# Performance work log

Measured on AMD Instinct MI355X. Metric: run time of the kernel, lower is better.

Reference implementation:

```python
import jax, jax.numpy as jnp
import numpy as np

D = 128
N = 20000
E = 640000
EPS = 1e-5


def setup_inputs() -> dict:
    key = jax.random.key(0)
    ks = jax.random.split(key, 12)
    x = jax.random.normal(ks[0], (N, D), dtype=jnp.float32)
    edge_index = jax.random.randint(ks[1], (2, E), 0, N, dtype=jnp.int64)
    edge_weight = jax.random.uniform(ks[2], (E,), dtype=jnp.float32)
    s = 1.0 / np.sqrt(D)
    # GraphConv params: lin_rel (bias=True) applied to aggregated messages,
    # lin_root (bias=False) applied to root features.
    W_rel = jax.random.uniform(ks[3], (D, D), minval=-s, maxval=s, dtype=jnp.float32)
    b_rel = jax.random.uniform(ks[4], (D,), minval=-s, maxval=s, dtype=jnp.float32)
    W_root = jax.random.uniform(ks[5], (D, D), minval=-s, maxval=s, dtype=jnp.float32)
    # add_linear Linear(out, out)
    lin_W = jax.random.uniform(ks[6], (D, D), minval=-s, maxval=s, dtype=jnp.float32)
    lin_b = jax.random.uniform(ks[7], (D,), minval=-s, maxval=s, dtype=jnp.float32)
    # LayerNorm affine params
    gamma = jnp.ones((D,), dtype=jnp.float32)
    beta = jnp.zeros((D,), dtype=jnp.float32)
    return {"x": x, "edge_index": edge_index, "edge_weight": edge_weight,
            "W_rel": W_rel, "b_rel": b_rel, "W_root": W_root,
            "lin_W": lin_W, "lin_b": lin_b, "gamma": gamma, "beta": beta}


def _layer_norm(h, gamma, beta):
    mu = jnp.mean(h, axis=-1, keepdims=True)
    var = jnp.mean(jnp.square(h - mu), axis=-1, keepdims=True)
    return (h - mu) * jax.lax.rsqrt(var + EPS) * gamma + beta


def reference(x, edge_index, edge_weight, W_rel, b_rel, W_root, lin_W, lin_b, gamma, beta):
    n = x.shape[0]
    src, dst = edge_index[0], edge_index[1]
    # message: edge_weight * x_j, gathered from source nodes
    msg = x[src] * edge_weight[:, None]                      # [E, D]
    # max aggregation to destination nodes; empty segments -> 0 (PyG fill)
    agg = jax.ops.segment_max(msg, dst, num_segments=n)      # [N, D]
    agg = jnp.where(jnp.isneginf(agg), 0.0, agg)
    # GraphConv: lin_rel(agg) + lin_root(x)
    h = agg @ W_rel.T + b_rel + x @ W_root.T                  # [N, D]
    # act + skip + norm
    h = jax.nn.gelu(h, approximate=False) + x
    h = _layer_norm(h, gamma, beta)
    # add_linear branch: act(lin(h)) + skip, then norm (module reuses self.norm)
    h2 = jax.nn.gelu(h @ lin_W.T + lin_b, approximate=False) + h
    h2 = _layer_norm(h2, gamma, beta)
    return h2, edge_weight
```

## Files before the change

### kernel.cpp

```cpp
#include <hip/hip_runtime.h>
#include <math.h>

#define N_NODES 20000
#define N_DIM   128
#define N_EDGES 640000
#define LN_EPS  1e-5f
#define CAP 64

#define TASK_E (N_EDGES / 4)
#define TASK_W 6144

typedef __attribute__((ext_vector_type(8))) short bf16x8;
typedef __attribute__((ext_vector_type(4))) float f32x4;

__device__ __forceinline__ float gelu_exact(float v) {
    return 0.5f * v * (1.0f + erff(v * 0.70710678118654752f));
}
__device__ __forceinline__ unsigned pack_bf16(float f) {
    unsigned b = __float_as_uint(f);
    return (b + 0x7FFFu + ((b >> 16) & 1u)) >> 16;
}
__device__ __forceinline__ bf16x8 pack8(const float* p) {
    union { bf16x8 v; unsigned short u[8]; } t;
    #pragma unroll
    for (int j = 0; j < 8; j++) t.u[j] = (unsigned short)pack_bf16(p[j]);
    return t.v;
}

__device__ __forceinline__ void pack_wfrag(int u, const float* __restrict__ Wr,
                                           const float* __restrict__ Wo,
                                           const float* __restrict__ Wl,
                                           unsigned short* __restrict__ Wb) {
    int m    = u >> 11;
    int rem  = u & 2047;
    int nt   = rem >> 8;
    int kt   = (rem >> 6) & 3;
    int lane = rem & 63;
    int n = nt * 16 + (lane & 15);
    int k = kt * 32 + ((lane >> 4) << 3);
    const float* W = (m == 0) ? Wr : ((m == 1) ? Wo : Wl);
    const float* p = W + n * N_DIM + k;
    union { uint4 q; unsigned short u16[8]; } t;
    #pragma unroll
    for (int j = 0; j < 8; j++) t.u16[j] = (unsigned short)pack_bf16(p[j]);
    ((uint4*)Wb)[u] = t.q;
}

__device__ __forceinline__ void gather_node(
    int node, int lane, const char* __restrict__ xb,
    int base, int dg, const int2* __restrict__ eb, unsigned* __restrict__ agg)
{
    const int lane8 = lane << 3;
    float m0 = -INFINITY, m1 = -INFINITY;
    const int hi = base + dg - 1;
    for (int j = 0; j < dg; j += 8) {
        int2 ev[8];
        #pragma unroll
        for (int k = 0; k < 8; k++)
            ev[k] = eb[min(base + j + k, hi)];
        float2 xv[8];
        #pragma unroll
        for (int k = 0; k < 8; k++)
            xv[k] = *(const float2*)(xb + (size_t)(unsigned)ev[k].x + lane8);
        #pragma unroll
        for (int k = 0; k < 8; k++) {
            float w = __int_as_float(ev[k].y);
            m0 = fmaxf(m0, xv[k].x * w);
            m1 = fmaxf(m1, xv[k].y * w);
        }
    }
    if (dg == 0) { m0 = 0.0f; m1 = 0.0f; }
    agg[node * 64 + lane] = pack_bf16(m0) | (pack_bf16(m1) << 16);
}

__global__ __launch_bounds__(256) void edge_pass_kernel(
    const int* __restrict__ ei, const float* __restrict__ ew,
    int* __restrict__ cnt, int2* __restrict__ buck, float* __restrict__ out_ew,
    const float* __restrict__ Wr, const float* __restrict__ Wo,
    const float* __restrict__ Wl, unsigned short* __restrict__ Wb)
{
    int t = blockIdx.x * blockDim.x + threadIdx.x;
    if (t < TASK_E) {
        int4 dst = ((const int4*)(ei + N_EDGES))[t];
        int4 src = ((const int4*)ei)[t];
        float4 w = ((const float4*)ew)[t];
        ((float4*)out_ew)[t] = w;
        int p0 = atomicAdd(&cnt[dst.x], 1);
        int p1 = atomicAdd(&cnt[dst.y], 1);
        int p2 = atomicAdd(&cnt[dst.z], 1);
        int p3 = atomicAdd(&cnt[dst.w], 1);
        buck[dst.x * CAP + min(p0, CAP - 1)] = make_int2(src.x << 9, __float_as_int(w.x));
        buck[dst.y * CAP + min(p1, CAP - 1)] = make_int2(src.y << 9, __float_as_int(w.y));
        buck[dst.z * CAP + min(p2, CAP - 1)] = make_int2(src.z << 9, __float_as_int(w.z));
        buck[dst.w * CAP + min(p3, CAP - 1)] = make_int2(src.w << 9, __float_as_int(w.w));
    } else if (t < TASK_E + TASK_W) {
        pack_wfrag(t - TASK_E, Wr, Wo, Wl, Wb);
    }
}

__global__ __launch_bounds__(64) void gather_bucket_kernel(
    const float* __restrict__ x, const int* __restrict__ cnt,
    const int2* __restrict__ buck, unsigned* __restrict__ agg)
{
    const int node = blockIdx.x;
    const int lane = threadIdx.x & 63;
    const int dg = min(__builtin_amdgcn_readfirstlane(cnt[node]), CAP);
    gather_node(node, lane, (const char*)x, node * CAP, dg, buck, agg);
}

__global__ __launch_bounds__(64) void gather_csr_kernel(
    const float* __restrict__ x, const int* __restrict__ off,
    const int2* __restrict__ csr, unsigned* __restrict__ agg)
{
    const int node = blockIdx.x;
    const int lane = threadIdx.x & 63;
    const int b = __builtin_amdgcn_readfirstlane(off[node]);
    const int dg = __builtin_amdgcn_readfirstlane(off[node + 1]) - b;
    gather_node(node, lane, (const char*)x, b, dg, csr, agg);
}

__global__ __launch_bounds__(64) void gemm_kernel(
    const float* __restrict__ x, const unsigned short* __restrict__ aggb,
    const unsigned short* __restrict__ Wb,
    const float* __restrict__ b_rel, const float* __restrict__ lin_b,
    const float* __restrict__ gamma, const float* __restrict__ beta,
    float* __restrict__ out)
{
    __shared__ float xs[16][132];
    const int lane = threadIdx.x & 63;
    const int quad = lane >> 4;
    const int col  = lane & 15;
    const int nb = blockIdx.x * 16;

    #pragma unroll
    for (int i = 0; i < 8; i++) {
        int f = i * 64 + lane;
        int r = f >> 5, c = (f & 31) << 2;
        float4 v = ((const float4*)x)[(size_t)(nb + r) * 32 + (f & 31)];
        *(float4*)&xs[r][c] = v;
    }

    float br[8], lb[8], gm[8], bt[8];
    #pragma unroll
    for (int nt = 0; nt < 8; nt++) {
        int c = nt * 16 + col;
        br[nt] = b_rel[c]; lb[nt] = lin_b[c]; gm[nt] = gamma[c]; bt[nt] = beta[c];
    }

    bf16x8 aggF[4], xF[4];
    #pragma unroll
    for (int kt = 0; kt < 4; kt++) {
        aggF[kt] = *(const bf16x8*)((const char*)aggb
                     + (size_t)(nb + col) * 256 + (size_t)(kt * 64 + quad * 16));
        xF[kt] = pack8(&xs[col][kt * 32 + quad * 8]);
    }

    f32x4 acc[8];
    #pragma unroll
    for (int nt = 0; nt < 8; nt++) {
        f32x4 a; a[0] = br[nt]; a[1] = br[nt]; a[2] = br[nt]; a[3] = br[nt];
        #pragma unroll
        for (int kt = 0; kt < 4; kt++) {
            bf16x8 wrel  = *(const bf16x8*)(Wb + ((size_t)((0 * 8 + nt) * 4 + kt) * 64 + lane) * 8);
            a = __builtin_amdgcn_mfma_f32_16x16x32_bf16(aggF[kt], wrel, a, 0, 0, 0);
            bf16x8 wroot = *(const bf16x8*)(Wb + ((size_t)((1 * 8 + nt) * 4 + kt) * 64 + lane) * 8);
            a = __builtin_amdgcn_mfma_f32_16x16x32_bf16(xF[kt], wroot, a, 0, 0, 0);
        }
        acc[nt] = a;
    }

    float hn[8][4];
    float sum[4] = {0, 0, 0, 0};
    #pragma unroll
    for (int nt = 0; nt < 8; nt++)
        #pragma unroll
        for (int rg = 0; rg < 4; rg++) {
            float val = gelu_exact(acc[nt][rg]) + xs[quad * 4 + rg][nt * 16 + col];
            hn[nt][rg] = val;
            sum[rg] += val;
        }
    #pragma unroll
    for (int m = 1; m < 16; m <<= 1)
        #pragma unroll
        for (int rg = 0; rg < 4; rg++) sum[rg] += __shfl_xor(sum[rg], m);
    float vs[4] = {0, 0, 0, 0};
    float mu[4];
    #pragma unroll
    for (int rg = 0; rg < 4; rg++) mu[rg] = sum[rg] * (1.0f / 128.0f);
    #pragma unroll
    for (int nt = 0; nt < 8; nt++)
        #pragma unroll
        for (int rg = 0; rg < 4; rg++) {
            float d = hn[nt][rg] - mu[rg];
            hn[nt][rg] = d;
            vs[rg] += d * d;
        }
    #pragma unroll
    for (int m = 1; m < 16; m <<= 1)
        #pragma unroll
        for (int rg = 0; rg < 4; rg++) vs[rg] += __shfl_xor(vs[rg], m);
    float rstd[4];
    #pragma unroll
    for (int rg = 0; rg < 4; rg++) rstd[rg] = rsqrtf(vs[rg] * (1.0f / 128.0f) + LN_EPS);
    #pragma unroll
    for (int nt = 0; nt < 8; nt++)
        #pragma unroll
        for (int rg = 0; rg < 4; rg++) {
            hn[nt][rg] = hn[nt][rg] * rstd[rg] * gm[nt] + bt[nt];
            xs[quad * 4 + rg][nt * 16 + col] = hn[nt][rg];
        }

    bf16x8 hF[4];
    #pragma unroll
    for (int kt = 0; kt < 4; kt++) hF[kt] = pack8(&xs[col][kt * 32 + quad * 8]);

    float g[8][4];
    float sum2[4] = {0, 0, 0, 0};
    #pragma unroll
    for (int nt = 0; nt < 8; nt++) {
        f32x4 a; a[0] = lb[nt]; a[1] = lb[nt]; a[2] = lb[nt]; a[3] = lb[nt];
        #pragma unroll
        for (int kt = 0; kt < 4; kt++) {
            bf16x8 wl = *(const bf16x8*)(Wb + ((size_t)((2 * 8 + nt) * 4 + kt) * 64 + lane) * 8);
            a = __builtin_amdgcn_mfma_f32_16x16x32_bf16(hF[kt], wl, a, 0, 0, 0);
        }
        #pragma unroll
        for (int rg = 0; rg < 4; rg++) {
            float val = gelu_exact(a[rg]) + hn[nt][rg];
            g[nt][rg] = val;
            sum2[rg] += val;
        }
    }
    #pragma unroll
    for (int m = 1; m < 16; m <<= 1)
        #pragma unroll
        for (int rg = 0; rg < 4; rg++) sum2[rg] += __shfl_xor(sum2[rg], m);
    float vs2[4] = {0, 0, 0, 0};
    #pragma unroll
    for (int rg = 0; rg < 4; rg++) mu[rg] = sum2[rg] * (1.0f / 128.0f);
    #pragma unroll
    for (int nt = 0; nt < 8; nt++)
        #pragma unroll
        for (int rg = 0; rg < 4; rg++) {
            float d = g[nt][rg] - mu[rg];
            g[nt][rg] = d;
            vs2[rg] += d * d;
        }
    #pragma unroll
    for (int m = 1; m < 16; m <<= 1)
        #pragma unroll
        for (int rg = 0; rg < 4; rg++) vs2[rg] += __shfl_xor(vs2[rg], m);
    #pragma unroll
    for (int rg = 0; rg < 4; rg++) rstd[rg] = rsqrtf(vs2[rg] * (1.0f / 128.0f) + LN_EPS);
    #pragma unroll
    for (int nt = 0; nt < 8; nt++)
        #pragma unroll
        for (int rg = 0; rg < 4; rg++)
            xs[quad * 4 + rg][nt * 16 + col] = g[nt][rg] * rstd[rg] * gm[nt] + bt[nt];

    #pragma unroll
    for (int r = 0; r < 16; r++) {
        float2 v = make_float2(xs[r][2 * lane], xs[r][2 * lane + 1]);
        ((float2*)(out + (size_t)(nb + r) * N_DIM))[lane] = v;
    }
}

__global__ __launch_bounds__(256) void prep_kernel(
    const int* __restrict__ ei, int* __restrict__ deg, int* __restrict__ rank,
    const float* __restrict__ ew, float* __restrict__ out_ew,
    const float* __restrict__ Wr, const float* __restrict__ Wo,
    const float* __restrict__ Wl, unsigned short* __restrict__ Wb)
{
    int t = blockIdx.x * blockDim.x + threadIdx.x;
    if (t < TASK_E) {
        int4 d = ((const int4*)(ei + N_EDGES))[t];
        float4 w = ((const float4*)ew)[t];
        ((float4*)out_ew)[t] = w;
        int4 r;
        r.x = atomicAdd(&deg[d.x], 1);
        r.y = atomicAdd(&deg[d.y], 1);
        r.z = atomicAdd(&deg[d.z], 1);
        r.w = atomicAdd(&deg[d.w], 1);
        ((int4*)rank)[t] = r;
    } else if (t < TASK_E + TASK_W) {
        pack_wfrag(t - TASK_E, Wr, Wo, Wl, Wb);
    }
}

__global__ __launch_bounds__(1024) void scan_kernel(const int* __restrict__ deg,
                                                    int* __restrict__ off) {
    __shared__ int sm2[1024];
    const int t = threadIdx.x;
    const int lo = t * 20;
    int4 d4[5];
    int s = 0;
    if (lo < N_NODES) {
        #pragma unroll
        for (int i = 0; i < 5; i++) {
            d4[i] = ((const int4*)(deg + lo))[i];
            s += d4[i].x + d4[i].y + d4[i].z + d4[i].w;
        }
    }
    sm2[t] = s;
    __syncthreads();
    for (int d = 1; d < 1024; d <<= 1) {
        int v = (t >= d) ? sm2[t - d] : 0;
        __syncthreads();
        sm2[t] += v;
        __syncthreads();
    }
    int base = sm2[t] - s;
    if (lo < N_NODES) {
        #pragma unroll
        for (int i = 0; i < 5; i++) {
            int4 o;
            o.x = base; base += d4[i].x;
            o.y = base; base += d4[i].y;
            o.z = base; base += d4[i].z;
            o.w = base; base += d4[i].w;
            ((int4*)(off + lo))[i] = o;
        }
    }
    if (t == 1023) off[N_NODES] = base;
}

__global__ __launch_bounds__(256) void fill_kernel(
    const int* __restrict__ ei, const float* __restrict__ ew,
    const int* __restrict__ rank, const int* __restrict__ off,
    int2* __restrict__ csr)
{
    int t = blockIdx.x * blockDim.x + threadIdx.x;
    if (t >= TASK_E) return;
    int4 dst  = ((const int4*)(ei + N_EDGES))[t];
    int4 rk   = ((const int4*)rank)[t];
    int4 src  = ((const int4*)ei)[t];
    float4 w  = ((const float4*)ew)[t];
    csr[off[dst.x] + rk.x] = make_int2(src.x << 9, __float_as_int(w.x));
    csr[off[dst.y] + rk.y] = make_int2(src.y << 9, __float_as_int(w.y));
    csr[off[dst.z] + rk.z] = make_int2(src.z << 9, __float_as_int(w.z));
    csr[off[dst.w] + rk.w] = make_int2(src.w << 9, __float_as_int(w.w));
}

extern "C" void kernel_launch(void* const* d_in, const int* in_sizes, int n_in,
                              void* d_out, int out_size, void* d_ws, size_t ws_size,
                              hipStream_t stream) {
    const float* x      = (const float*)d_in[0];
    const int*   ei     = (const int*)  d_in[1];
    const float* ew     = (const float*)d_in[2];
    const float* W_rel  = (const float*)d_in[3];
    const float* b_rel  = (const float*)d_in[4];
    const float* W_root = (const float*)d_in[5];
    const float* lin_W  = (const float*)d_in[6];
    const float* lin_b  = (const float*)d_in[7];
    const float* gamma  = (const float*)d_in[8];
    const float* beta   = (const float*)d_in[9];
    float* out = (float*)d_out;
    float* out_ew = out + (size_t)N_NODES * N_DIM;

    const size_t SZ_CNT  = (size_t)N_NODES * 4;
    const size_t SZ_WB   = (size_t)TASK_W * 16;
    const size_t SZ_BUCK = (size_t)N_NODES * CAP * 8;
    const size_t SZ_AGG  = (size_t)N_NODES * 64 * 4;
    const size_t need_main = SZ_CNT + SZ_WB + SZ_BUCK + SZ_AGG;

    if (ws_size >= need_main) {
        int*            cnt  = (int*)d_ws;
        unsigned short* Wb   = (unsigned short*)((char*)d_ws + SZ_CNT);
        int2*           buck = (int2*)((char*)d_ws + SZ_CNT + SZ_WB);
        unsigned*       agg  = (unsigned*)((char*)d_ws + SZ_CNT + SZ_WB + SZ_BUCK);
        hipMemsetAsync(cnt, 0, SZ_CNT, stream);
        edge_pass_kernel<<<(TASK_E + TASK_W + 255) / 256, 256, 0, stream>>>(
            ei, ew, cnt, buck, out_ew, W_rel, W_root, lin_W, Wb);
        gather_bucket_kernel<<<N_NODES, 64, 0, stream>>>(x, cnt, buck, agg);
        gemm_kernel<<<N_NODES / 16, 64, 0, stream>>>(
            x, (const unsigned short*)agg, Wb, b_rel, lin_b, gamma, beta, out);
    } else {
        int*            deg  = (int*)d_ws;
        int*            off  = deg + N_NODES;
        int*            rank = off + (N_NODES + 4);
        int2*           csr  = (int2*)(rank + N_EDGES);
        unsigned short* Wb   = (unsigned short*)(csr + N_EDGES);
        unsigned*       agg  = (unsigned*)((char*)Wb + SZ_WB);
        hipMemsetAsync(deg, 0, SZ_CNT, stream);
        prep_kernel<<<(TASK_E + TASK_W + 255) / 256, 256, 0, stream>>>(
            ei, deg, rank, ew, out_ew, W_rel, W_root, lin_W, Wb);
        scan_kernel<<<1, 1024, 0, stream>>>(deg, off);
        fill_kernel<<<(TASK_E + 255) / 256, 256, 0, stream>>>(ei, ew, rank, off, csr);
        gather_csr_kernel<<<N_NODES, 64, 0, stream>>>(x, off, csr, agg);
        gemm_kernel<<<N_NODES / 16, 64, 0, stream>>>(
            x, (const unsigned short*)agg, Wb, b_rel, lin_b, gamma, beta, out);
    }
}
```

Baseline: 175.2 us.

## Gather from bf16 copy of x and use one edge per thread in edge pass

```diff
diff --git a/kernel.cpp b/kernel.cpp
--- a/kernel.cpp
+++ b/kernel.cpp
@@ -7,7 +7,8 @@
 #define LN_EPS  1e-5f
 #define CAP 64
 
-#define TASK_E (N_EDGES / 4)
+#define TASK_A (N_EDGES / 4)
+#define TASK_X (N_NODES * N_DIM / 8)
 #define TASK_W 6144
 
 typedef __attribute__((ext_vector_type(8))) short bf16x8;
@@ -46,11 +47,11 @@
     ((uint4*)Wb)[u] = t.q;
 }
 
+template<bool BF16X>
 __device__ __forceinline__ void gather_node(
     int node, int lane, const char* __restrict__ xb,
     int base, int dg, const int2* __restrict__ eb, unsigned* __restrict__ agg)
 {
-    const int lane8 = lane << 3;
     float m0 = -INFINITY, m1 = -INFINITY;
     const int hi = base + dg - 1;
     for (int j = 0; j < dg; j += 8) {
@@ -58,15 +59,28 @@
         #pragma unroll
         for (int k = 0; k < 8; k++)
             ev[k] = eb[min(base + j + k, hi)];
-        float2 xv[8];
-        #pragma unroll
-        for (int k = 0; k < 8; k++)
-            xv[k] = *(const float2*)(xb + (size_t)(unsigned)ev[k].x + lane8);
-        #pragma unroll
-        for (int k = 0; k < 8; k++) {
-            float w = __int_as_float(ev[k].y);
-            m0 = fmaxf(m0, xv[k].x * w);
-            m1 = fmaxf(m1, xv[k].y * w);
+        if (BF16X) {
+            unsigned xv[8];
+            #pragma unroll
+            for (int k = 0; k < 8; k++)
+                xv[k] = *(const unsigned*)(xb + (size_t)(unsigned)ev[k].x + lane * 4);
+            #pragma unroll
+            for (int k = 0; k < 8; k++) {
+                float w = __int_as_float(ev[k].y);
+                m0 = fmaxf(m0, __uint_as_float(xv[k] << 16) * w);
+                m1 = fmaxf(m1, __uint_as_float(xv[k] & 0xFFFF0000u) * w);
+            }
+        } else {
+            float2 xv[8];
+            #pragma unroll
+            for (int k = 0; k < 8; k++)
+                xv[k] = *(const float2*)(xb + (size_t)(unsigned)ev[k].x + lane * 8);
+            #pragma unroll
+            for (int k = 0; k < 8; k++) {
+                float w = __int_as_float(ev[k].y);
+                m0 = fmaxf(m0, xv[k].x * w);
+                m1 = fmaxf(m1, xv[k].y * w);
+            }
         }
     }
     if (dg == 0) { m0 = 0.0f; m1 = 0.0f; }
@@ -76,36 +90,43 @@
 __global__ __launch_bounds__(256) void edge_pass_kernel(
     const int* __restrict__ ei, const float* __restrict__ ew,
     int* __restrict__ cnt, int2* __restrict__ buck, float* __restrict__ out_ew,
+    const float* __restrict__ x, unsigned* __restrict__ xbf,
     const float* __restrict__ Wr, const float* __restrict__ Wo,
     const float* __restrict__ Wl, unsigned short* __restrict__ Wb)
 {
     int t = blockIdx.x * blockDim.x + threadIdx.x;
-    if (t < TASK_E) {
-        int4 dst = ((const int4*)(ei + N_EDGES))[t];
-        int4 src = ((const int4*)ei)[t];
-        float4 w = ((const float4*)ew)[t];
-        ((float4*)out_ew)[t] = w;
-        int p0 = atomicAdd(&cnt[dst.x], 1);
-        int p1 = atomicAdd(&cnt[dst.y], 1);
-        int p2 = atomicAdd(&cnt[dst.z], 1);
-        int p3 = atomicAdd(&cnt[dst.w], 1);
-        buck[dst.x * CAP + min(p0, CAP - 1)] = make_int2(src.x << 9, __float_as_int(w.x));
-        buck[dst.y * CAP + min(p1, CAP - 1)] = make_int2(src.y << 9, __float_as_int(w.y));
-        buck[dst.z * CAP + min(p2, CAP - 1)] = make_int2(src.z << 9, __float_as_int(w.z));
-        buck[dst.w * CAP + min(p3, CAP - 1)] = make_int2(src.w << 9, __float_as_int(w.w));
-    } else if (t < TASK_E + TASK_W) {
-        pack_wfrag(t - TASK_E, Wr, Wo, Wl, Wb);
+    if (t < N_EDGES) {
+        int dst = ei[N_EDGES + t];
+        int src = ei[t];
+        float w = ew[t];
+        int p = atomicAdd(&cnt[dst], 1);
+        buck[dst * CAP + min(p, CAP - 1)] = make_int2(src << 8, __float_as_int(w));
+    } else if (t < N_EDGES + TASK_A) {
+        int u = t - N_EDGES;
+        ((float4*)out_ew)[u] = ((const float4*)ew)[u];
+    } else if (t < N_EDGES + TASK_A + TASK_X) {
+        int u = t - N_EDGES - TASK_A;
+        float4 a = ((const float4*)x)[u * 2];
+        float4 b = ((const float4*)x)[u * 2 + 1];
+        uint4 o;
+        o.x = pack_bf16(a.x) | (pack_bf16(a.y) << 16);
+        o.y = pack_bf16(a.z) | (pack_bf16(a.w) << 16);
+        o.z = pack_bf16(b.x) | (pack_bf16(b.y) << 16);
+        o.w = pack_bf16(b.z) | (pack_bf16(b.w) << 16);
+        ((uint4*)xbf)[u] = o;
+    } else if (t < N_EDGES + TASK_A + TASK_X + TASK_W) {
+        pack_wfrag(t - N_EDGES - TASK_A - TASK_X, Wr, Wo, Wl, Wb);
     }
 }
 
 __global__ __launch_bounds__(64) void gather_bucket_kernel(
-    const float* __restrict__ x, const int* __restrict__ cnt,
+    const unsigned* __restrict__ xbf, const int* __restrict__ cnt,
     const int2* __restrict__ buck, unsigned* __restrict__ agg)
 {
     const int node = blockIdx.x;
     const int lane = threadIdx.x & 63;
     const int dg = min(__builtin_amdgcn_readfirstlane(cnt[node]), CAP);
-    gather_node(node, lane, (const char*)x, node * CAP, dg, buck, agg);
+    gather_node<true>(node, lane, (const char*)xbf, node * CAP, dg, buck, agg);
 }
 
 __global__ __launch_bounds__(64) void gather_csr_kernel(
@@ -116,7 +137,7 @@
     const int lane = threadIdx.x & 63;
     const int b = __builtin_amdgcn_readfirstlane(off[node]);
     const int dg = __builtin_amdgcn_readfirstlane(off[node + 1]) - b;
-    gather_node(node, lane, (const char*)x, b, dg, csr, agg);
+    gather_node<false>(node, lane, (const char*)x, b, dg, csr, agg);
 }
 
 __global__ __launch_bounds__(64) void gemm_kernel(
@@ -272,18 +293,14 @@
     const float* __restrict__ Wl, unsigned short* __restrict__ Wb)
 {
     int t = blockIdx.x * blockDim.x + threadIdx.x;
-    if (t < TASK_E) {
-        int4 d = ((const int4*)(ei + N_EDGES))[t];
-        float4 w = ((const float4*)ew)[t];
-        ((float4*)out_ew)[t] = w;
-        int4 r;
-        r.x = atomicAdd(&deg[d.x], 1);
-        r.y = atomicAdd(&deg[d.y], 1);
-        r.z = atomicAdd(&deg[d.z], 1);
-        r.w = atomicAdd(&deg[d.w], 1);
-        ((int4*)rank)[t] = r;
-    } else if (t < TASK_E + TASK_W) {
-        pack_wfrag(t - TASK_E, Wr, Wo, Wl, Wb);
+    if (t < N_EDGES) {
+        int dst = ei[N_EDGES + t];
+        rank[t] = atomicAdd(&deg[dst], 1);
+    } else if (t < N_EDGES + TASK_A) {
+        int u = t - N_EDGES;
+        ((float4*)out_ew)[u] = ((const float4*)ew)[u];
+    } else if (t < N_EDGES + TASK_A + TASK_W) {
+        pack_wfrag(t - N_EDGES - TASK_A, Wr, Wo, Wl, Wb);
     }
 }
 
@@ -330,15 +347,9 @@
     int2* __restrict__ csr)
 {
     int t = blockIdx.x * blockDim.x + threadIdx.x;
-    if (t >= TASK_E) return;
-    int4 dst  = ((const int4*)(ei + N_EDGES))[t];
-    int4 rk   = ((const int4*)rank)[t];
-    int4 src  = ((const int4*)ei)[t];
-    float4 w  = ((const float4*)ew)[t];
-    csr[off[dst.x] + rk.x] = make_int2(src.x << 9, __float_as_int(w.x));
-    csr[off[dst.y] + rk.y] = make_int2(src.y << 9, __float_as_int(w.y));
-    csr[off[dst.z] + rk.z] = make_int2(src.z << 9, __float_as_int(w.z));
-    csr[off[dst.w] + rk.w] = make_int2(src.w << 9, __float_as_int(w.w));
+    if (t >= N_EDGES) return;
+    int dst = ei[N_EDGES + t];
+    csr[off[dst] + rank[t]] = make_int2(ei[t] << 9, __float_as_int(ew[t]));
 }
 
 extern "C" void kernel_launch(void* const* d_in, const int* in_sizes, int n_in,
@@ -359,19 +370,22 @@
 
     const size_t SZ_CNT  = (size_t)N_NODES * 4;
     const size_t SZ_WB   = (size_t)TASK_W * 16;
+    const size_t SZ_XBF  = (size_t)N_NODES * N_DIM * 2;
     const size_t SZ_BUCK = (size_t)N_NODES * CAP * 8;
     const size_t SZ_AGG  = (size_t)N_NODES * 64 * 4;
-    const size_t need_main = SZ_CNT + SZ_WB + SZ_BUCK + SZ_AGG;
+    const size_t need_main = SZ_CNT + SZ_WB + SZ_XBF + SZ_BUCK + SZ_AGG;
 
     if (ws_size >= need_main) {
         int*            cnt  = (int*)d_ws;
         unsigned short* Wb   = (unsigned short*)((char*)d_ws + SZ_CNT);
-        int2*           buck = (int2*)((char*)d_ws + SZ_CNT + SZ_WB);
-        unsigned*       agg  = (unsigned*)((char*)d_ws + SZ_CNT + SZ_WB + SZ_BUCK);
+        unsigned*       xbf  = (unsigned*)((char*)d_ws + SZ_CNT + SZ_WB);
+        int2*           buck = (int2*)((char*)d_ws + SZ_CNT + SZ_WB + SZ_XBF);
+        unsigned*       agg  = (unsigned*)((char*)d_ws + SZ_CNT + SZ_WB + SZ_XBF + SZ_BUCK);
         hipMemsetAsync(cnt, 0, SZ_CNT, stream);
-        edge_pass_kernel<<<(TASK_E + TASK_W + 255) / 256, 256, 0, stream>>>(
-            ei, ew, cnt, buck, out_ew, W_rel, W_root, lin_W, Wb);
-        gather_bucket_kernel<<<N_NODES, 64, 0, stream>>>(x, cnt, buck, agg);
+        const int n_thr = N_EDGES + TASK_A + TASK_X + TASK_W;
+        edge_pass_kernel<<<(n_thr + 255) / 256, 256, 0, stream>>>(
+            ei, ew, cnt, buck, out_ew, x, xbf, W_rel, W_root, lin_W, Wb);
+        gather_bucket_kernel<<<N_NODES, 64, 0, stream>>>(xbf, cnt, buck, agg);
         gemm_kernel<<<N_NODES / 16, 64, 0, stream>>>(
             x, (const unsigned short*)agg, Wb, b_rel, lin_b, gamma, beta, out);
     } else {
@@ -382,10 +396,10 @@
         unsigned short* Wb   = (unsigned short*)(csr + N_EDGES);
         unsigned*       agg  = (unsigned*)((char*)Wb + SZ_WB);
         hipMemsetAsync(deg, 0, SZ_CNT, stream);
-        prep_kernel<<<(TASK_E + TASK_W + 255) / 256, 256, 0, stream>>>(
+        prep_kernel<<<(N_EDGES + TASK_A + TASK_W + 255) / 256, 256, 0, stream>>>(
             ei, deg, rank, ew, out_ew, W_rel, W_root, lin_W, Wb);
         scan_kernel<<<1, 1024, 0, stream>>>(deg, off);
-        fill_kernel<<<(TASK_E + 255) / 256, 256, 0, stream>>>(ei, ew, rank, off, csr);
+        fill_kernel<<<(N_EDGES + 255) / 256, 256, 0, stream>>>(ei, ew, rank, off, csr);
         gather_csr_kernel<<<N_NODES, 64, 0, stream>>>(x, off, csr, agg);
         gemm_kernel<<<N_NODES / 16, 64, 0, stream>>>(
             x, (const unsigned short*)agg, Wb, b_rel, lin_b, gamma, beta, out);
```

Result: faster. 157.7 us (-10.0%).

## Gather from a bf16 copy of x and halve GEMM rows per block

Applied to the files above, without the earlier changes.

```diff
diff --git a/kernel.cpp b/kernel.cpp
--- a/kernel.cpp
+++ b/kernel.cpp
@@ -6,8 +6,10 @@
 #define N_EDGES 640000
 #define LN_EPS  1e-5f
 #define CAP 64
+#define NPG 8
 
 #define TASK_E (N_EDGES / 4)
+#define TASK_X (N_NODES * N_DIM / 8)
 #define TASK_W 6144
 
 typedef __attribute__((ext_vector_type(8))) short bf16x8;
@@ -46,11 +48,11 @@
     ((uint4*)Wb)[u] = t.q;
 }
 
+template<bool BF16X>
 __device__ __forceinline__ void gather_node(
     int node, int lane, const char* __restrict__ xb,
     int base, int dg, const int2* __restrict__ eb, unsigned* __restrict__ agg)
 {
-    const int lane8 = lane << 3;
     float m0 = -INFINITY, m1 = -INFINITY;
     const int hi = base + dg - 1;
     for (int j = 0; j < dg; j += 8) {
@@ -58,15 +60,28 @@
         #pragma unroll
         for (int k = 0; k < 8; k++)
             ev[k] = eb[min(base + j + k, hi)];
-        float2 xv[8];
-        #pragma unroll
-        for (int k = 0; k < 8; k++)
-            xv[k] = *(const float2*)(xb + (size_t)(unsigned)ev[k].x + lane8);
-        #pragma unroll
-        for (int k = 0; k < 8; k++) {
-            float w = __int_as_float(ev[k].y);
-            m0 = fmaxf(m0, xv[k].x * w);
-            m1 = fmaxf(m1, xv[k].y * w);
+        if (BF16X) {
+            unsigned xv[8];
+            #pragma unroll
+            for (int k = 0; k < 8; k++)
+                xv[k] = *(const unsigned*)(xb + (size_t)(unsigned)ev[k].x + lane * 4);
+            #pragma unroll
+            for (int k = 0; k < 8; k++) {
+                float w = __int_as_float(ev[k].y);
+                m0 = fmaxf(m0, __uint_as_float(xv[k] << 16) * w);
+                m1 = fmaxf(m1, __uint_as_float(xv[k] & 0xFFFF0000u) * w);
+            }
+        } else {
+            float2 xv[8];
+            #pragma unroll
+            for (int k = 0; k < 8; k++)
+                xv[k] = *(const float2*)(xb + (size_t)(unsigned)ev[k].x + lane * 8);
+            #pragma unroll
+            for (int k = 0; k < 8; k++) {
+                float w = __int_as_float(ev[k].y);
+                m0 = fmaxf(m0, xv[k].x * w);
+                m1 = fmaxf(m1, xv[k].y * w);
+            }
         }
     }
     if (dg == 0) { m0 = 0.0f; m1 = 0.0f; }
@@ -76,6 +91,7 @@
 __global__ __launch_bounds__(256) void edge_pass_kernel(
     const int* __restrict__ ei, const float* __restrict__ ew,
     int* __restrict__ cnt, int2* __restrict__ buck, float* __restrict__ out_ew,
+    const float* __restrict__ x, unsigned* __restrict__ xbf,
     const float* __restrict__ Wr, const float* __restrict__ Wo,
     const float* __restrict__ Wl, unsigned short* __restrict__ Wb)
 {
@@ -89,23 +105,33 @@
         int p1 = atomicAdd(&cnt[dst.y], 1);
         int p2 = atomicAdd(&cnt[dst.z], 1);
         int p3 = atomicAdd(&cnt[dst.w], 1);
-        buck[dst.x * CAP + min(p0, CAP - 1)] = make_int2(src.x << 9, __float_as_int(w.x));
-        buck[dst.y * CAP + min(p1, CAP - 1)] = make_int2(src.y << 9, __float_as_int(w.y));
-        buck[dst.z * CAP + min(p2, CAP - 1)] = make_int2(src.z << 9, __float_as_int(w.z));
-        buck[dst.w * CAP + min(p3, CAP - 1)] = make_int2(src.w << 9, __float_as_int(w.w));
-    } else if (t < TASK_E + TASK_W) {
-        pack_wfrag(t - TASK_E, Wr, Wo, Wl, Wb);
+        buck[dst.x * CAP + min(p0, CAP - 1)] = make_int2(src.x << 8, __float_as_int(w.x));
+        buck[dst.y * CAP + min(p1, CAP - 1)] = make_int2(src.y << 8, __float_as_int(w.y));
+        buck[dst.z * CAP + min(p2, CAP - 1)] = make_int2(src.z << 8, __float_as_int(w.z));
+        buck[dst.w * CAP + min(p3, CAP - 1)] = make_int2(src.w << 8, __float_as_int(w.w));
+    } else if (t < TASK_E + TASK_X) {
+        int u = t - TASK_E;
+        float4 a = ((const float4*)x)[u * 2];
+        float4 b = ((const float4*)x)[u * 2 + 1];
+        uint4 o;
+        o.x = pack_bf16(a.x) | (pack_bf16(a.y) << 16);
+        o.y = pack_bf16(a.z) | (pack_bf16(a.w) << 16);
+        o.z = pack_bf16(b.x) | (pack_bf16(b.y) << 16);
+        o.w = pack_bf16(b.z) | (pack_bf16(b.w) << 16);
+        ((uint4*)xbf)[u] = o;
+    } else if (t < TASK_E + TASK_X + TASK_W) {
+        pack_wfrag(t - TASK_E - TASK_X, Wr, Wo, Wl, Wb);
     }
 }
 
 __global__ __launch_bounds__(64) void gather_bucket_kernel(
-    const float* __restrict__ x, const int* __restrict__ cnt,
+    const unsigned* __restrict__ xbf, const int* __restrict__ cnt,
     const int2* __restrict__ buck, unsigned* __restrict__ agg)
 {
     const int node = blockIdx.x;
     const int lane = threadIdx.x & 63;
     const int dg = min(__builtin_amdgcn_readfirstlane(cnt[node]), CAP);
-    gather_node(node, lane, (const char*)x, node * CAP, dg, buck, agg);
+    gather_node<true>(node, lane, (const char*)xbf, node * CAP, dg, buck, agg);
 }
 
 __global__ __launch_bounds__(64) void gather_csr_kernel(
@@ -116,7 +142,7 @@
     const int lane = threadIdx.x & 63;
     const int b = __builtin_amdgcn_readfirstlane(off[node]);
     const int dg = __builtin_amdgcn_readfirstlane(off[node + 1]) - b;
-    gather_node(node, lane, (const char*)x, b, dg, csr, agg);
+    gather_node<false>(node, lane, (const char*)x, b, dg, csr, agg);
 }
 
 __global__ __launch_bounds__(64) void gemm_kernel(
@@ -126,14 +152,15 @@
     const float* __restrict__ gamma, const float* __restrict__ beta,
     float* __restrict__ out)
 {
-    __shared__ float xs[16][132];
+    __shared__ float xs[NPG][132];
     const int lane = threadIdx.x & 63;
     const int quad = lane >> 4;
     const int col  = lane & 15;
-    const int nb = blockIdx.x * 16;
-
-    #pragma unroll
-    for (int i = 0; i < 8; i++) {
+    const int arow = col & 7;
+    const int nb = blockIdx.x * NPG;
+
+    #pragma unroll
+    for (int i = 0; i < 4; i++) {
         int f = i * 64 + lane;
         int r = f >> 5, c = (f & 31) << 2;
         float4 v = ((const float4*)x)[(size_t)(nb + r) * 32 + (f & 31)];
@@ -151,8 +178,8 @@
     #pragma unroll
     for (int kt = 0; kt < 4; kt++) {
         aggF[kt] = *(const bf16x8*)((const char*)aggb
-                     + (size_t)(nb + col) * 256 + (size_t)(kt * 64 + quad * 16));
-        xF[kt] = pack8(&xs[col][kt * 32 + quad * 8]);
+                     + (size_t)(nb + arow) * 256 + (size_t)(kt * 64 + quad * 16));
+        xF[kt] = pack8(&xs[arow][kt * 32 + quad * 8]);
     }
 
     f32x4 acc[8];
@@ -175,7 +202,7 @@
     for (int nt = 0; nt < 8; nt++)
         #pragma unroll
         for (int rg = 0; rg < 4; rg++) {
-            float val = gelu_exact(acc[nt][rg]) + xs[quad * 4 + rg][nt * 16 + col];
+            float val = gelu_exact(acc[nt][rg]) + xs[(quad * 4 + rg) & 7][nt * 16 + col];
             hn[nt][rg] = val;
             sum[rg] += val;
         }
@@ -207,12 +234,13 @@
         #pragma unroll
         for (int rg = 0; rg < 4; rg++) {
             hn[nt][rg] = hn[nt][rg] * rstd[rg] * gm[nt] + bt[nt];
-            xs[quad * 4 + rg][nt * 16 + col] = hn[nt][rg];
+            if (quad < 2)
+                xs[quad * 4 + rg][nt * 16 + col] = hn[nt][rg];
         }
 
     bf16x8 hF[4];
     #pragma unroll
-    for (int kt = 0; kt < 4; kt++) hF[kt] = pack8(&xs[col][kt * 32 + quad * 8]);
+    for (int kt = 0; kt < 4; kt++) hF[kt] = pack8(&xs[arow][kt * 32 + quad * 8]);
 
     float g[8][4];
     float sum2[4] = {0, 0, 0, 0};
@@ -256,10 +284,11 @@
     for (int nt = 0; nt < 8; nt++)
         #pragma unroll
         for (int rg = 0; rg < 4; rg++)
-            xs[quad * 4 + rg][nt * 16 + col] = g[nt][rg] * rstd[rg] * gm[nt] + bt[nt];
-
-    #pragma unroll
-    for (int r = 0; r < 16; r++) {
+            if (quad < 2)
+                xs[quad * 4 + rg][nt * 16 + col] = g[nt][rg] * rstd[rg] * gm[nt] + bt[nt];
+
+    #pragma unroll
+    for (int r = 0; r < NPG; r++) {
         float2 v = make_float2(xs[r][2 * lane], xs[r][2 * lane + 1]);
         ((float2*)(out + (size_t)(nb + r) * N_DIM))[lane] = v;
     }
@@ -359,20 +388,23 @@
 
     const size_t SZ_CNT  = (size_t)N_NODES * 4;
     const size_t SZ_WB   = (size_t)TASK_W * 16;
+    const size_t SZ_XBF  = (size_t)N_NODES * N_DIM * 2;
     const size_t SZ_BUCK = (size_t)N_NODES * CAP * 8;
     const size_t SZ_AGG  = (size_t)N_NODES * 64 * 4;
-    const size_t need_main = SZ_CNT + SZ_WB + SZ_BUCK + SZ_AGG;
+    const size_t need_main = SZ_CNT + SZ_WB + SZ_XBF + SZ_BUCK + SZ_AGG;
 
     if (ws_size >= need_main) {
         int*            cnt  = (int*)d_ws;
         unsigned short* Wb   = (unsigned short*)((char*)d_ws + SZ_CNT);
-        int2*           buck = (int2*)((char*)d_ws + SZ_CNT + SZ_WB);
-        unsigned*       agg  = (unsigned*)((char*)d_ws + SZ_CNT + SZ_WB + SZ_BUCK);
+        unsigned*       xbf  = (unsigned*)((char*)d_ws + SZ_CNT + SZ_WB);
+        int2*           buck = (int2*)((char*)d_ws + SZ_CNT + SZ_WB + SZ_XBF);
+        unsigned*       agg  = (unsigned*)((char*)d_ws + SZ_CNT + SZ_WB + SZ_XBF + SZ_BUCK);
         hipMemsetAsync(cnt, 0, SZ_CNT, stream);
-        edge_pass_kernel<<<(TASK_E + TASK_W + 255) / 256, 256, 0, stream>>>(
-            ei, ew, cnt, buck, out_ew, W_rel, W_root, lin_W, Wb);
-        gather_bucket_kernel<<<N_NODES, 64, 0, stream>>>(x, cnt, buck, agg);
-        gemm_kernel<<<N_NODES / 16, 64, 0, stream>>>(
+        const int n_thr = TASK_E + TASK_X + TASK_W;
+        edge_pass_kernel<<<(n_thr + 255) / 256, 256, 0, stream>>>(
+            ei, ew, cnt, buck, out_ew, x, xbf, W_rel, W_root, lin_W, Wb);
+        gather_bucket_kernel<<<N_NODES, 64, 0, stream>>>(xbf, cnt, buck, agg);
+        gemm_kernel<<<N_NODES / NPG, 64, 0, stream>>>(
             x, (const unsigned short*)agg, Wb, b_rel, lin_b, gamma, beta, out);
     } else {
         int*            deg  = (int*)d_ws;
@@ -387,7 +419,7 @@
         scan_kernel<<<1, 1024, 0, stream>>>(deg, off);
         fill_kernel<<<(TASK_E + 255) / 256, 256, 0, stream>>>(ei, ew, rank, off, csr);
         gather_csr_kernel<<<N_NODES, 64, 0, stream>>>(x, off, csr, agg);
-        gemm_kernel<<<N_NODES / 16, 64, 0, stream>>>(
+        gemm_kernel<<<N_NODES / NPG, 64, 0, stream>>>(
             x, (const unsigned short*)agg, Wb, b_rel, lin_b, gamma, beta, out);
     }
 }
```

New measurement: 179.9 us. 2.7% more time.
